# Kernel tuning notes

Measured on AMD Instinct MI355X. Metric: run time of the kernel, lower is better.

The kernel has to match this reference:

```python
import jax, jax.numpy as jnp
import numpy as np

N = 50000      # nodes
E = 800000     # edges (avg degree 16)
D = 512        # in_features
H = 512        # gcn hidden dim (both layers)
G = 64         # graphs in batch
C = 10         # num_classes


def setup_inputs() -> dict:
    key = jax.random.key(0)
    ks = jax.random.split(key, 12)
    x = jax.random.normal(ks[0], (N, D), dtype=jnp.float32)
    edge_index = jax.random.randint(ks[1], (2, E), 0, N, dtype=jnp.int64)
    batch = jnp.sort(jax.random.randint(ks[2], (N,), 0, G, dtype=jnp.int64))
    w = lambda k, sh: (jax.random.normal(k, sh, dtype=jnp.float32) * 0.02)
    return {
        "x": x,
        "edge_index": edge_index,
        "batch": batch,
        # GraphConv layer 0: lin_rel (weight+bias) applied to aggregated neighbors,
        # lin_root (weight, no bias) applied to self features.
        "Wr0": w(ks[3], (D, H)), "br0": jnp.zeros((H,), jnp.float32), "Ws0": w(ks[4], (D, H)),
        # GraphConv layer 1
        "Wr1": w(ks[5], (H, H)), "br1": jnp.zeros((H,), jnp.float32), "Ws1": w(ks[6], (H, H)),
        # final Linear
        "Wl": w(ks[7], (H, C)), "bl": jnp.zeros((C,), jnp.float32),
    }


def _graph_conv(x, src, dst, Wr, br, Ws):
    # sum-aggregate neighbor features: agg[i] = sum_{(j->i) in E} x[j]
    agg = jax.ops.segment_sum(x[src], dst, num_segments=N)  # [N, d_in]
    return agg @ Wr + br + x @ Ws                           # [N, d_out]


def reference(x, edge_index, batch, Wr0, br0, Ws0, Wr1, br1, Ws1, Wl, bl):
    src, dst = edge_index[0], edge_index[1]
    h = jax.nn.relu(_graph_conv(x, src, dst, Wr0, br0, Ws0))   # dropout = identity (eval)
    h = jax.nn.relu(_graph_conv(h, src, dst, Wr1, br1, Ws1))
    # global mean pool over graphs
    sums = jax.ops.segment_sum(h, batch, num_segments=G)                       # [G, H]
    counts = jax.ops.segment_sum(jnp.ones((N, 1), h.dtype), batch, num_segments=G)
    pooled = jax.nn.relu(sums / jnp.maximum(counts, 1.0))
    return pooled @ Wl + bl  # [G, C]
```

## Files before the change

### kernel.cpp

```cpp
#include <hip/hip_runtime.h>

#define NN 50000
#define NE 800000
#define MP 50048
#define GG 64
#define HD 512
#define K2 1024
#define SCAN_BLKS 196

typedef __attribute__((ext_vector_type(8))) short bf16x8;
typedef __attribute__((ext_vector_type(4))) float f32x4;

__device__ __forceinline__ unsigned short f2bf(float f) {
  unsigned u = __builtin_bit_cast(unsigned, f);
  u += 0x7fffu + ((u >> 16) & 1u);
  return (unsigned short)(u >> 16);
}
__device__ __forceinline__ float bf2f(unsigned short h) {
  unsigned u = ((unsigned)h) << 16;
  return __builtin_bit_cast(float, u);
}

__device__ __forceinline__ void g2l16(const void* g, void* l) {
  __builtin_amdgcn_global_load_lds(
      (const __attribute__((address_space(1))) unsigned int*)g,
      (__attribute__((address_space(3))) unsigned int*)l, 16, 0, 0);
}

__global__ void wt_kernel(const float* __restrict__ Wr, const float* __restrict__ Ws,
                          unsigned short* __restrict__ Wt) {
  int idx = blockIdx.x * 256 + threadIdx.x;
  if (idx >= HD * K2) return;
  int n = idx >> 10;
  int k = idx & (K2 - 1);
  float v = (k < HD) ? Wr[k * HD + n] : Ws[(k - HD) * HD + n];
  Wt[idx] = f2bf(v);
}

__global__ void cvtpad_kernel(const float* __restrict__ in, unsigned short* __restrict__ out,
                              int rows_in, long long total4) {
  long long i = (long long)blockIdx.x * 256 + threadIdx.x;
  for (; i < total4; i += (long long)gridDim.x * 256) {
    int r = (int)((i * 4) >> 9);
    float4 v = make_float4(0.f, 0.f, 0.f, 0.f);
    if (r < rows_in) v = ((const float4*)in)[i];
    ushort4 o;
    o.x = f2bf(v.x); o.y = f2bf(v.y); o.z = f2bf(v.z); o.w = f2bf(v.w);
    ((ushort4*)out)[i] = o;
  }
}

__global__ void hist_kernel(const int* __restrict__ ei, int* __restrict__ deg) {
  int i = blockIdx.x * 256 + threadIdx.x;
  if (i < NE) atomicAdd(&deg[ei[NE + i]], 1);
}

__global__ __launch_bounds__(256) void scan1_kernel(const int* __restrict__ deg,
                                                    int* __restrict__ tmp,
                                                    int* __restrict__ bsum) {
  __shared__ int sh[256];
  int t = threadIdx.x;
  int i = blockIdx.x * 256 + t;
  int v = (i < NN) ? deg[i] : 0;
  sh[t] = v;
  __syncthreads();
#pragma unroll
  for (int off = 1; off < 256; off <<= 1) {
    int u = (t >= off) ? sh[t - off] : 0;
    __syncthreads();
    sh[t] += u;
    __syncthreads();
  }
  if (i < NN) tmp[i] = sh[t] - v;
  if (t == 255) bsum[blockIdx.x] = sh[255];
}

__global__ __launch_bounds__(256) void scan2_kernel(int* __restrict__ bsum,
                                                    int* __restrict__ row_ptr) {
  __shared__ int sh[256];
  int t = threadIdx.x;
  int v = (t < SCAN_BLKS) ? bsum[t] : 0;
  sh[t] = v;
  __syncthreads();
#pragma unroll
  for (int off = 1; off < 256; off <<= 1) {
    int u = (t >= off) ? sh[t - off] : 0;
    __syncthreads();
    sh[t] += u;
    __syncthreads();
  }
  if (t < SCAN_BLKS) bsum[t] = sh[t] - v;
  if (t == 255) row_ptr[NN] = sh[255];
}

__global__ __launch_bounds__(256) void scan3_kernel(const int* __restrict__ tmp,
                                                    const int* __restrict__ bsum,
                                                    int* __restrict__ row_ptr,
                                                    int* __restrict__ cursor) {
  int i = blockIdx.x * 256 + threadIdx.x;
  if (i < NN) {
    int r = tmp[i] + bsum[blockIdx.x];
    row_ptr[i] = r;
    cursor[i] = r;
  }
}

__global__ void fill_kernel(const int* __restrict__ ei, int* __restrict__ cursor,
                            int* __restrict__ col) {
  int i = blockIdx.x * 256 + threadIdx.x;
  if (i < NE) {
    int d = ei[NE + i];
    int p = atomicAdd(&cursor[d], 1);
    col[p] = ei[i];
  }
}

__global__ __launch_bounds__(256) void gather_kernel(const unsigned short* __restrict__ X,
                                                     const int* __restrict__ row_ptr,
                                                     const int* __restrict__ col,
                                                     unsigned short* __restrict__ out) {
  int w = (blockIdx.x * 256 + threadIdx.x) >> 6;
  int lane = threadIdx.x & 63;
  if (w >= MP) return;
  float a0 = 0.f, a1 = 0.f, a2 = 0.f, a3 = 0.f, a4 = 0.f, a5 = 0.f, a6 = 0.f, a7 = 0.f;
  if (w < NN) {
    int r0 = row_ptr[w], r1 = row_ptr[w + 1];
    for (int base = r0; base < r1; base += 64) {
      int idx = base + lane;
      int myc = (idx < r1) ? col[idx] : 0;
      int cnt = min(64, r1 - base);
      #pragma unroll 8
      for (int j = 0; j < cnt; j++) {
        int c = __shfl(myc, j);
        uint4 v = *(const uint4*)(X + (size_t)c * HD + lane * 8);
        a0 += bf2f((unsigned short)(v.x & 0xffff));
        a1 += bf2f((unsigned short)(v.x >> 16));
        a2 += bf2f((unsigned short)(v.y & 0xffff));
        a3 += bf2f((unsigned short)(v.y >> 16));
        a4 += bf2f((unsigned short)(v.z & 0xffff));
        a5 += bf2f((unsigned short)(v.z >> 16));
        a6 += bf2f((unsigned short)(v.w & 0xffff));
        a7 += bf2f((unsigned short)(v.w >> 16));
      }
    }
  }
  uint4 o;
  o.x = ((unsigned)f2bf(a1) << 16) | f2bf(a0);
  o.y = ((unsigned)f2bf(a3) << 16) | f2bf(a2);
  o.z = ((unsigned)f2bf(a5) << 16) | f2bf(a4);
  o.w = ((unsigned)f2bf(a7) << 16) | f2bf(a6);
  *(uint4*)(out + (size_t)w * HD + lane * 8) = o;
}

__global__ __launch_bounds__(512, 2) void gemm_kernel(
    const unsigned short* __restrict__ A0, const unsigned short* __restrict__ A1,
    const unsigned short* __restrict__ Wt, const float* __restrict__ bias,
    unsigned short* __restrict__ Hout) {
  __shared__ __align__(16) unsigned short Ads[128 * 64];
  __shared__ __align__(16) unsigned short Bds[256 * 64];

  const int tid = threadIdx.x;
  const int lane = tid & 63;
  const int wv = tid >> 6;
  const int wm = wv >> 2;
  const int wn = wv & 3;

  const int nwg = 782;
  const int orig = blockIdx.x;
  const int q = nwg >> 3, r8 = nwg & 7;
  const int xcd = orig & 7;
  const int wgid = (xcd < r8 ? xcd * (q + 1) : r8 * (q + 1) + (xcd - r8) * q) + (orig >> 3);

  const int mt = wgid >> 1;
  const int nt = wgid & 1;
  const int row0 = mt * 128;
  const int col0 = nt * 256;

  f32x4 acc[4][4];
#pragma unroll
  for (int i = 0; i < 4; i++)
#pragma unroll
    for (int j = 0; j < 4; j++) acc[i][j] = (f32x4)(0.f);

  const int lr = lane >> 3;
  const int lc = lane & 7;
  const int csw = lc ^ lr;

  for (int kt = 0; kt < 16; ++kt) {
    const int k0 = kt * 64;
    const unsigned short* Asrc = (k0 < HD) ? A0 : A1;
    const int ka = k0 & (HD - 1);
#pragma unroll
    for (int it = 0; it < 2; ++it) {
      int rg = it * 8 + wv;
      g2l16(Asrc + (size_t)(row0 + rg * 8 + lr) * HD + ka + csw * 8, &Ads[rg * 8 * 64]);
    }
#pragma unroll
    for (int it = 0; it < 4; ++it) {
      int rg = it * 8 + wv;
      g2l16(Wt + (size_t)(col0 + rg * 8 + lr) * K2 + k0 + csw * 8, &Bds[rg * 8 * 64]);
    }
    __syncthreads();
#pragma unroll
    for (int kk = 0; kk < 2; ++kk) {
      bf16x8 af[4], bfr[4];
#pragma unroll
      for (int m = 0; m < 4; m++) {
        int r = wm * 64 + m * 16 + (lane & 15);
        int ck = (kk * 4 + (lane >> 4)) ^ (r & 7);
        af[m] = *(const bf16x8*)&Ads[r * 64 + ck * 8];
      }
#pragma unroll
      for (int n = 0; n < 4; n++) {
        int r = wn * 64 + n * 16 + (lane & 15);
        int ck = (kk * 4 + (lane >> 4)) ^ (r & 7);
        bfr[n] = *(const bf16x8*)&Bds[r * 64 + ck * 8];
      }
#pragma unroll
      for (int m = 0; m < 4; m++)
#pragma unroll
        for (int n = 0; n < 4; n++)
          acc[m][n] = __builtin_amdgcn_mfma_f32_16x16x32_bf16(af[m], bfr[n], acc[m][n], 0, 0, 0);
    }
    __syncthreads();
  }

#pragma unroll
  for (int n = 0; n < 4; n++) {
    int c = col0 + wn * 64 + n * 16 + (lane & 15);
    float bv = bias[c];
#pragma unroll
    for (int m = 0; m < 4; m++) {
      int rbase = row0 + wm * 64 + m * 16 + (lane >> 4) * 4;
#pragma unroll
      for (int r = 0; r < 4; r++) {
        float v = acc[m][n][r] + bv;
        v = v > 0.f ? v : 0.f;
        Hout[(size_t)(rbase + r) * HD + c] = f2bf(v);
      }
    }
  }
}

__device__ __forceinline__ int lbound(const int* b, int v) {
  int lo = 0, hi = NN;
  while (lo < hi) { int m = (lo + hi) >> 1; if (b[m] < v) lo = m + 1; else hi = m; }
  return lo;
}

__global__ void pool_kernel(const unsigned short* __restrict__ H, const int* __restrict__ batch,
                            float* __restrict__ pooled) {
  int b = blockIdx.x;
  int g = b >> 4;
  int half = (b >> 3) & 1;
  int chunk = b & 7;
  int col = half * 256 + threadIdx.x;
  int start = lbound(batch, g);
  int end = lbound(batch, g + 1);
  int len = end - start;
  int r0 = start + (int)(((long long)len * chunk) >> 3);
  int r1 = start + (int)(((long long)len * (chunk + 1)) >> 3);
  float s = 0.f;
  for (int r = r0; r < r1; r++) s += bf2f(H[(size_t)r * HD + col]);
  atomicAdd(&pooled[g * HD + col], s);
}

__global__ void final_kernel(const float* __restrict__ pooled, const int* __restrict__ batch,
                             const float* __restrict__ Wl, const float* __restrict__ bl,
                             float* __restrict__ out) {
  int g = blockIdx.x;
  int t = threadIdx.x;
  int lane = t & 63, wv = t >> 6;
  int start = lbound(batch, g);
  int end = lbound(batch, g + 1);
  float cnt = (float)(end - start);
  if (cnt < 1.f) cnt = 1.f;
  float a[10];
#pragma unroll
  for (int c = 0; c < 10; c++) a[c] = 0.f;
  for (int n = t; n < HD; n += 256) {
    float p = pooled[g * HD + n] / cnt;
    p = p > 0.f ? p : 0.f;
#pragma unroll
    for (int c = 0; c < 10; c++) a[c] += p * Wl[n * 10 + c];
  }
  __shared__ float red[10][4];
#pragma unroll
  for (int c = 0; c < 10; c++) {
    float v = a[c];
#pragma unroll
    for (int off = 32; off >= 1; off >>= 1) v += __shfl_down(v, off);
    if (lane == 0) red[c][wv] = v;
  }
  __syncthreads();
  if (t < 10) out[g * 10 + t] = red[t][0] + red[t][1] + red[t][2] + red[t][3] + bl[t];
}

extern "C" void kernel_launch(void* const* d_in, const int* in_sizes, int n_in,
                              void* d_out, int out_size, void* d_ws, size_t ws_size,
                              hipStream_t stream) {
  const float* x   = (const float*)d_in[0];
  const int* ei    = (const int*)d_in[1];
  const int* batch = (const int*)d_in[2];
  const float* Wr0 = (const float*)d_in[3];
  const float* br0 = (const float*)d_in[4];
  const float* Ws0 = (const float*)d_in[5];
  const float* Wr1 = (const float*)d_in[6];
  const float* br1 = (const float*)d_in[7];
  const float* Ws1 = (const float*)d_in[8];
  const float* Wl  = (const float*)d_in[9];
  const float* bl  = (const float*)d_in[10];
  float* out = (float*)d_out;

  char* ws = (char*)d_ws;
  size_t off = 0;
  auto alloc = [&](size_t bytes) { char* p = ws + off; off += (bytes + 255) & ~255ULL; return p; };
  unsigned short* xb   = (unsigned short*)alloc((size_t)MP * HD * 2);
  unsigned short* h0   = (unsigned short*)alloc((size_t)MP * HD * 2);
  unsigned short* aggb = (unsigned short*)alloc((size_t)MP * HD * 2);
  unsigned short* Wt0  = (unsigned short*)alloc((size_t)HD * K2 * 2);
  unsigned short* Wt1  = (unsigned short*)alloc((size_t)HD * K2 * 2);
  float* pooled        = (float*)alloc((size_t)GG * HD * 4);
  int* deg             = (int*)alloc((size_t)NN * 4);
  int* row_ptr         = (int*)alloc((size_t)(NN + 1) * 4);
  int* cursor          = (int*)alloc((size_t)NN * 4);
  int* col             = (int*)alloc((size_t)NE * 4);
  int* stmp            = (int*)alloc((size_t)NN * 4);
  int* bsum            = (int*)alloc((size_t)256 * 4);
  unsigned short* h1 = xb;

  const long long totMP4 = (long long)MP * HD / 4;

  hipMemsetAsync(deg, 0, (size_t)NN * 4, stream);
  hist_kernel<<<(NE + 255) / 256, 256, 0, stream>>>(ei, deg);
  scan1_kernel<<<SCAN_BLKS, 256, 0, stream>>>(deg, stmp, bsum);
  scan2_kernel<<<1, 256, 0, stream>>>(bsum, row_ptr);
  scan3_kernel<<<SCAN_BLKS, 256, 0, stream>>>(stmp, bsum, row_ptr, cursor);
  fill_kernel<<<(NE + 255) / 256, 256, 0, stream>>>(ei, cursor, col);

  wt_kernel<<<2048, 256, 0, stream>>>(Wr0, Ws0, Wt0);
  wt_kernel<<<2048, 256, 0, stream>>>(Wr1, Ws1, Wt1);
  cvtpad_kernel<<<2048, 256, 0, stream>>>(x, xb, NN, totMP4);

  gather_kernel<<<MP / 4, 256, 0, stream>>>(xb, row_ptr, col, aggb);
  gemm_kernel<<<391 * 2, 512, 0, stream>>>(aggb, xb, Wt0, br0, h0);

  gather_kernel<<<MP / 4, 256, 0, stream>>>(h0, row_ptr, col, aggb);
  gemm_kernel<<<391 * 2, 512, 0, stream>>>(aggb, h0, Wt1, br1, h1);

  hipMemsetAsync(pooled, 0, (size_t)GG * HD * 4, stream);
  pool_kernel<<<GG * 16, 256, 0, stream>>>(h1, batch, pooled);
  final_kernel<<<GG, 256, 0, stream>>>(pooled, batch, Wl, bl, out);
}
```

Baseline: 667.6 us.

## Fuse preprocessing kernels into one launch and batch gather loads by eight

Merges the two weight-transpose kernels, the x conversion/padding kernel and the degree histogram into a single prep_kernel that dispatches on block index. The weight transpose now goes through an LDS tile, so both reads and writes are coalesced. The gather inner loop issues eight neighbor row loads before accumulating, which exposes more memory-level parallelism. This cuts launch count and the uncoalesced transpose writes, at the cost of a more complex heterogeneous kernel and higher register pressure in the gather.

After: 662.4 us. Within noise of the previous version (-0.8%).

```diff
diff --git a/kernel.cpp b/kernel.cpp
--- a/kernel.cpp
+++ b/kernel.cpp
@@ -27,32 +27,49 @@
       (__attribute__((address_space(3))) unsigned int*)l, 16, 0, 0);
 }
 
-__global__ void wt_kernel(const float* __restrict__ Wr, const float* __restrict__ Ws,
-                          unsigned short* __restrict__ Wt) {
-  int idx = blockIdx.x * 256 + threadIdx.x;
-  if (idx >= HD * K2) return;
-  int n = idx >> 10;
-  int k = idx & (K2 - 1);
-  float v = (k < HD) ? Wr[k * HD + n] : Ws[(k - HD) * HD + n];
-  Wt[idx] = f2bf(v);
-}
-
-__global__ void cvtpad_kernel(const float* __restrict__ in, unsigned short* __restrict__ out,
-                              int rows_in, long long total4) {
-  long long i = (long long)blockIdx.x * 256 + threadIdx.x;
-  for (; i < total4; i += (long long)gridDim.x * 256) {
-    int r = (int)((i * 4) >> 9);
-    float4 v = make_float4(0.f, 0.f, 0.f, 0.f);
-    if (r < rows_in) v = ((const float4*)in)[i];
-    ushort4 o;
-    o.x = f2bf(v.x); o.y = f2bf(v.y); o.z = f2bf(v.z); o.w = f2bf(v.w);
-    ((ushort4*)out)[i] = o;
-  }
-}
-
-__global__ void hist_kernel(const int* __restrict__ ei, int* __restrict__ deg) {
-  int i = blockIdx.x * 256 + threadIdx.x;
-  if (i < NE) atomicAdd(&deg[ei[NE + i]], 1);
+__global__ __launch_bounds__(256) void prep_kernel(
+    const float* __restrict__ x, unsigned short* __restrict__ xb,
+    const float* __restrict__ Wr0, const float* __restrict__ Ws0, unsigned short* __restrict__ Wt0,
+    const float* __restrict__ Wr1, const float* __restrict__ Ws1, unsigned short* __restrict__ Wt1,
+    const int* __restrict__ ei, int* __restrict__ deg) {
+  int b = blockIdx.x, t = threadIdx.x;
+  if (b < 256) {
+    __shared__ float sh[64][65];
+    int layer = b >> 7, tl = b & 127;
+    int tn = tl >> 4, tk = tl & 15;
+    int half = tk >> 3;
+    int kw = (tk & 7) * 64, n0 = tn * 64;
+    const float* W = layer ? (half ? Ws1 : Wr1) : (half ? Ws0 : Wr0);
+    unsigned short* Wt = layer ? Wt1 : Wt0;
+    int nn = t & 63;
+    int kb = t >> 6;
+#pragma unroll
+    for (int i = 0; i < 16; i++) {
+      int kk = kb + i * 4;
+      sh[kk][nn] = W[(size_t)(kw + kk) * HD + n0 + nn];
+    }
+    __syncthreads();
+    int kk2 = t & 63;
+#pragma unroll
+    for (int i = 0; i < 16; i++) {
+      int nn2 = kb + i * 4;
+      Wt[(size_t)(n0 + nn2) * K2 + half * HD + kw + kk2] = f2bf(sh[kk2][nn2]);
+    }
+  } else if (b < 2304) {
+    const long long total4 = (long long)MP * HD / 4;
+    for (long long i = (long long)(b - 256) * 256 + t; i < total4; i += 2048LL * 256) {
+      int r = (int)((i * 4) >> 9);
+      float4 v = make_float4(0.f, 0.f, 0.f, 0.f);
+      if (r < NN) v = ((const float4*)x)[i];
+      ushort4 o;
+      o.x = f2bf(v.x); o.y = f2bf(v.y); o.z = f2bf(v.z); o.w = f2bf(v.w);
+      ((ushort4*)xb)[i] = o;
+    }
+  } else {
+    for (int i = (b - 2304) * 256 + t; i < NE; i += 512 * 256) {
+      atomicAdd(&deg[ei[NE + i]], 1);
+    }
+  }
 }
 
 __global__ __launch_bounds__(256) void scan1_kernel(const int* __restrict__ deg,
@@ -115,6 +132,16 @@
   }
 }
 
+#define ACC8(v, a)                                        \
+  a[0] += bf2f((unsigned short)((v).x & 0xffff));         \
+  a[1] += bf2f((unsigned short)((v).x >> 16));            \
+  a[2] += bf2f((unsigned short)((v).y & 0xffff));         \
+  a[3] += bf2f((unsigned short)((v).y >> 16));            \
+  a[4] += bf2f((unsigned short)((v).z & 0xffff));         \
+  a[5] += bf2f((unsigned short)((v).z >> 16));            \
+  a[6] += bf2f((unsigned short)((v).w & 0xffff));         \
+  a[7] += bf2f((unsigned short)((v).w >> 16));
+
 __global__ __launch_bounds__(256) void gather_kernel(const unsigned short* __restrict__ X,
                                                      const int* __restrict__ row_ptr,
                                                      const int* __restrict__ col,
@@ -122,33 +149,43 @@
   int w = (blockIdx.x * 256 + threadIdx.x) >> 6;
   int lane = threadIdx.x & 63;
   if (w >= MP) return;
-  float a0 = 0.f, a1 = 0.f, a2 = 0.f, a3 = 0.f, a4 = 0.f, a5 = 0.f, a6 = 0.f, a7 = 0.f;
+  float a[8] = {0.f, 0.f, 0.f, 0.f, 0.f, 0.f, 0.f, 0.f};
   if (w < NN) {
     int r0 = row_ptr[w], r1 = row_ptr[w + 1];
+    const unsigned short* Xl = X + lane * 8;
     for (int base = r0; base < r1; base += 64) {
       int idx = base + lane;
       int myc = (idx < r1) ? col[idx] : 0;
       int cnt = min(64, r1 - base);
-      #pragma unroll 8
-      for (int j = 0; j < cnt; j++) {
+      int j = 0;
+      for (; j + 8 <= cnt; j += 8) {
+        int c0 = __shfl(myc, j + 0), c1 = __shfl(myc, j + 1);
+        int c2 = __shfl(myc, j + 2), c3 = __shfl(myc, j + 3);
+        int c4 = __shfl(myc, j + 4), c5 = __shfl(myc, j + 5);
+        int c6 = __shfl(myc, j + 6), c7 = __shfl(myc, j + 7);
+        uint4 v0 = *(const uint4*)(Xl + (size_t)c0 * HD);
+        uint4 v1 = *(const uint4*)(Xl + (size_t)c1 * HD);
+        uint4 v2 = *(const uint4*)(Xl + (size_t)c2 * HD);
+        uint4 v3 = *(const uint4*)(Xl + (size_t)c3 * HD);
+        uint4 v4 = *(const uint4*)(Xl + (size_t)c4 * HD);
+        uint4 v5 = *(const uint4*)(Xl + (size_t)c5 * HD);
+        uint4 v6 = *(const uint4*)(Xl + (size_t)c6 * HD);
+        uint4 v7 = *(const uint4*)(Xl + (size_t)c7 * HD);
+        ACC8(v0, a) ACC8(v1, a) ACC8(v2, a) ACC8(v3, a)
+        ACC8(v4, a) ACC8(v5, a) ACC8(v6, a) ACC8(v7, a)
+      }
+      for (; j < cnt; j++) {
         int c = __shfl(myc, j);
-        uint4 v = *(const uint4*)(X + (size_t)c * HD + lane * 8);
-        a0 += bf2f((unsigned short)(v.x & 0xffff));
-        a1 += bf2f((unsigned short)(v.x >> 16));
-        a2 += bf2f((unsigned short)(v.y & 0xffff));
-        a3 += bf2f((unsigned short)(v.y >> 16));
-        a4 += bf2f((unsigned short)(v.z & 0xffff));
-        a5 += bf2f((unsigned short)(v.z >> 16));
-        a6 += bf2f((unsigned short)(v.w & 0xffff));
-        a7 += bf2f((unsigned short)(v.w >> 16));
+        uint4 v = *(const uint4*)(Xl + (size_t)c * HD);
+        ACC8(v, a)
       }
     }
   }
   uint4 o;
-  o.x = ((unsigned)f2bf(a1) << 16) | f2bf(a0);
-  o.y = ((unsigned)f2bf(a3) << 16) | f2bf(a2);
-  o.z = ((unsigned)f2bf(a5) << 16) | f2bf(a4);
-  o.w = ((unsigned)f2bf(a7) << 16) | f2bf(a6);
+  o.x = ((unsigned)f2bf(a[1]) << 16) | f2bf(a[0]);
+  o.y = ((unsigned)f2bf(a[3]) << 16) | f2bf(a[2]);
+  o.z = ((unsigned)f2bf(a[5]) << 16) | f2bf(a[4]);
+  o.w = ((unsigned)f2bf(a[7]) << 16) | f2bf(a[6]);
   *(uint4*)(out + (size_t)w * HD + lane * 8) = o;
 }
 
@@ -329,26 +366,22 @@
   int* bsum            = (int*)alloc((size_t)256 * 4);
   unsigned short* h1 = xb;
 
-  const long long totMP4 = (long long)MP * HD / 4;
-
   hipMemsetAsync(deg, 0, (size_t)NN * 4, stream);
-  hist_kernel<<<(NE + 255) / 256, 256, 0, stream>>>(ei, deg);
+  hipMemsetAsync(pooled, 0, (size_t)GG * HD * 4, stream);
+
+  prep_kernel<<<2816, 256, 0, stream>>>(x, xb, Wr0, Ws0, Wt0, Wr1, Ws1, Wt1, ei, deg);
+
   scan1_kernel<<<SCAN_BLKS, 256, 0, stream>>>(deg, stmp, bsum);
   scan2_kernel<<<1, 256, 0, stream>>>(bsum, row_ptr);
   scan3_kernel<<<SCAN_BLKS, 256, 0, stream>>>(stmp, bsum, row_ptr, cursor);
   fill_kernel<<<(NE + 255) / 256, 256, 0, stream>>>(ei, cursor, col);
 
-  wt_kernel<<<2048, 256, 0, stream>>>(Wr0, Ws0, Wt0);
-  wt_kernel<<<2048, 256, 0, stream>>>(Wr1, Ws1, Wt1);
-  cvtpad_kernel<<<2048, 256, 0, stream>>>(x, xb, NN, totMP4);
-
   gather_kernel<<<MP / 4, 256, 0, stream>>>(xb, row_ptr, col, aggb);
-  gemm_kernel<<<391 * 2, 512, 0, stream>>>(aggb, xb, Wt0, br0, h0);
+  gemm_kernel<<<782, 512, 0, stream>>>(aggb, xb, Wt0, br0, h0);
 
   gather_kernel<<<MP / 4, 256, 0, stream>>>(h0, row_ptr, col, aggb);
-  gemm_kernel<<<391 * 2, 512, 0, stream>>>(aggb, h0, Wt1, br1, h1);
-
-  hipMemsetAsync(pooled, 0, (size_t)GG * HD * 4, stream);
+  gemm_kernel<<<782, 512, 0, stream>>>(aggb, h0, Wt1, br1, h1);
+
   pool_kernel<<<GG * 16, 256, 0, stream>>>(h1, batch, pooled);
   final_kernel<<<GG, 256, 0, stream>>>(pooled, batch, Wl, bl, out);
 }
```
